# Kernel optimization log

Measured on AMD Instinct MI355X. Metric: run time of the kernel, lower is better.

## Reference

```python
import jax, jax.numpy as jnp
import numpy as np
from jax import lax

T = 256          # sentence length
WD, TD = 300, 100  # word/tag embedding dims
H = WD + TD      # LSTM hidden (=input) size, per module __init__
VOCAB, NTAGS = 50000, 50
MLP_H = 400


def setup_inputs() -> dict:
    key = jax.random.key(0)
    ks = jax.random.split(key, 20)
    s = 0.05  # small init scale for numerical stability
    return {
        "words": jax.random.randint(ks[0], (T,), 0, VOCAB),
        "tags": jax.random.randint(ks[1], (T,), 0, NTAGS),
        "word_emb": jax.random.normal(ks[2], (VOCAB, WD), jnp.float32),
        "tag_emb": jax.random.normal(ks[3], (NTAGS, TD), jnp.float32),
        "Wih0": jax.random.normal(ks[4], (2, 4 * H, H), jnp.float32) * s,
        "Whh0": jax.random.normal(ks[5], (2, 4 * H, H), jnp.float32) * s,
        "bih0": jax.random.normal(ks[6], (2, 4 * H), jnp.float32) * s,
        "bhh0": jax.random.normal(ks[7], (2, 4 * H), jnp.float32) * s,
        "Wih1": jax.random.normal(ks[8], (2, 4 * H, 2 * H), jnp.float32) * s,
        "Whh1": jax.random.normal(ks[9], (2, 4 * H, H), jnp.float32) * s,
        "bih1": jax.random.normal(ks[10], (2, 4 * H), jnp.float32) * s,
        "bhh1": jax.random.normal(ks[11], (2, 4 * H), jnp.float32) * s,
        "W1": jax.random.normal(ks[12], (MLP_H, 4 * H), jnp.float32) * s,
        "b1": jax.random.normal(ks[13], (MLP_H,), jnp.float32) * s,
        "W2": jax.random.normal(ks[14], (1, MLP_H), jnp.float32) * s,
        "b2": jax.random.normal(ks[15], (1,), jnp.float32) * s,
        "h0": jax.random.normal(ks[16], (2, 2, H), jnp.float32),  # [layer, dir, H]
        "c0": jax.random.normal(ks[17], (2, 2, H), jnp.float32),
    }


def _lstm_dir(xs, Wih, Whh, bih, bhh, h0, c0, reverse):
    # xs: [T, D]; torch LSTM gate order i, f, g, o
    def step(carry, xt):
        h, c = carry
        g = xt @ Wih.T + bih + h @ Whh.T + bhh  # [4H]
        i, f, gg, o = jnp.split(g, 4)
        c = jax.nn.sigmoid(f) * c + jax.nn.sigmoid(i) * jnp.tanh(gg)
        h = jax.nn.sigmoid(o) * jnp.tanh(c)
        return (h, c), h
    _, hs = lax.scan(step, (h0, c0), xs, reverse=reverse)
    return hs  # [T, H]


def _forward(words, tags, word_emb, tag_emb, Wih0, Whh0, bih0, bhh0,
             Wih1, Whh1, bih1, bhh1, W1, b1, W2, b2, h0, c0):
    x = jnp.concatenate([word_emb[words], tag_emb[tags]], axis=1)  # [T, H]
    # layer 0, both directions
    hf0 = _lstm_dir(x, Wih0[0], Whh0[0], bih0[0], bhh0[0], h0[0, 0], c0[0, 0], False)
    hb0 = _lstm_dir(x, Wih0[1], Whh0[1], bih0[1], bhh0[1], h0[0, 1], c0[0, 1], True)
    x1 = jnp.concatenate([hf0, hb0], axis=1)  # [T, 2H]
    # layer 1
    hf1 = _lstm_dir(x1, Wih1[0], Whh1[0], bih1[0], bhh1[0], h0[1, 0], c0[1, 0], False)
    hb1 = _lstm_dir(x1, Wih1[1], Whh1[1], bih1[1], bhh1[1], h0[1, 1], c0[1, 1], True)
    hvec = jnp.concatenate([hf1, hb1], axis=1)  # [T, 2H]
    # batched pairwise MLP: score(i,j) = W2 @ tanh(W1 @ [h_i; h_j] + b1) + b2
    # Split W1 so the concat is never materialized over all T^2 pairs.
    W1a, W1b = W1[:, :2 * H], W1[:, 2 * H:]
    pi = hvec @ W1a.T  # [T, MLP_H] contribution of head word i
    pj = hvec @ W1b.T  # [T, MLP_H] contribution of dependent word j
    act = jnp.tanh(pi[:, None, :] + pj[None, :, :] + b1)  # [T, T, MLP_H]
    scores = act @ W2[0] + b2[0]  # [T, T]
    # diagonal stays 0 (permutations exclude i == j; scoreTensor was zeroed)
    return scores * (1.0 - jnp.eye(T, dtype=scores.dtype))


def reference(words, tags, word_emb, tag_emb, Wih0, Whh0, bih0, bhh0,
              Wih1, Whh1, bih1, bhh1, W1, b1, W2, b2, h0, c0):
    return _forward(words, tags, word_emb, tag_emb, Wih0, Whh0, bih0, bhh0,
                    Wih1, Whh1, bih1, bhh1, W1, b1, W2, b2, h0, c0)
```

## Files before the change

kernel.cpp:

```cpp
#include <hip/hip_runtime.h>
#include <hip/hip_bf16.h>

#define T 256
#define H 400
#define G4 1600
#define WD 300
#define TD 100
#define MLP_H 400
#define NBLK_D 25
#define HB 16
#define GR 64
#define WSTR 202
#define NPAIR 200

typedef _Float16 f16;
typedef _Float16 half2t __attribute__((ext_vector_type(2)));
typedef unsigned long long u64;
typedef unsigned int u32;

__device__ __forceinline__ float fexp(float x) {
    return __builtin_amdgcn_exp2f(x * 1.4426950408889634f);
}
__device__ __forceinline__ float sigf(float x) {
    return __builtin_amdgcn_rcpf(1.0f + fexp(-x));
}
__device__ __forceinline__ float tanhf_fast(float x) {
    return 1.0f - 2.0f * __builtin_amdgcn_rcpf(1.0f + fexp(2.0f * x));
}
__device__ __forceinline__ unsigned short f16bits(f16 x) {
    union { f16 h; unsigned short u; } v; v.h = x; return v.u;
}
__device__ __forceinline__ u32 packh2(float a, float b) {
    half2t hv; hv.x = (_Float16)a; hv.y = (_Float16)b;
    return __builtin_bit_cast(u32, hv);
}

#if __has_builtin(__builtin_amdgcn_fdot2)
__device__ __forceinline__ float dot2u(u32 a, u32 b, float c) {
    return __builtin_amdgcn_fdot2(__builtin_bit_cast(half2t, a),
                                  __builtin_bit_cast(half2t, b), c, false);
}
#else
__device__ __forceinline__ float dot2u(u32 a, u32 b, float c) {
    half2t x = __builtin_bit_cast(half2t, a), y = __builtin_bit_cast(half2t, b);
    return fmaf((float)x.y, (float)y.y, fmaf((float)x.x, (float)y.x, c));
}
#endif

__device__ __forceinline__ u64 sysload(const u64* p) {
    return __hip_atomic_load(p, __ATOMIC_RELAXED, __HIP_MEMORY_SCOPE_SYSTEM);
}
__device__ __forceinline__ void sysstore(u64* p, u64 v) {
    __hip_atomic_store(p, v, __ATOMIC_RELAXED, __HIP_MEMORY_SCOPE_SYSTEM);
}

__global__ void gather_k(const int* __restrict__ words, const int* __restrict__ tags,
                         const float* __restrict__ wemb, const float* __restrict__ temb,
                         float* __restrict__ x0) {
    int t = blockIdx.x;
    int w = words[t], g = tags[t];
    for (int c = threadIdx.x; c < H; c += 128) {
        float v = (c < WD) ? wemb[w * WD + c] : temb[g * TD + (c - WD)];
        x0[t * H + c] = v;
    }
}

__global__ __launch_bounds__(256) void gemm_tn(
    const float* __restrict__ X, int ldx,
    const float* __restrict__ Wt, int ldw, int wofs,
    const float* __restrict__ bias1, const float* __restrict__ bias2,
    float* __restrict__ out, int ldo, int Rt, int K) {
    __shared__ float Xs[64][17];
    __shared__ float Ws[64][17];
    const int tid = threadIdx.x;
    const int t0 = blockIdx.x * 64, r0 = blockIdx.y * 64;
    const int lr = tid >> 2, kq = (tid & 3) * 4;
    const int ti = tid >> 4, rj = tid & 15;
    float acc[4][4] = {};
    for (int k0 = 0; k0 < K; k0 += 16) {
        float4 xv = *(const float4*)(X + (size_t)(t0 + lr) * ldx + k0 + kq);
        Xs[lr][kq + 0] = xv.x; Xs[lr][kq + 1] = xv.y;
        Xs[lr][kq + 2] = xv.z; Xs[lr][kq + 3] = xv.w;
        int r = r0 + lr;
        float4 wv = make_float4(0.f, 0.f, 0.f, 0.f);
        if (r < Rt) wv = *(const float4*)(Wt + (size_t)r * ldw + wofs + k0 + kq);
        Ws[lr][kq + 0] = wv.x; Ws[lr][kq + 1] = wv.y;
        Ws[lr][kq + 2] = wv.z; Ws[lr][kq + 3] = wv.w;
        __syncthreads();
#pragma unroll
        for (int k = 0; k < 16; k++) {
            float xr[4], wr[4];
#pragma unroll
            for (int m = 0; m < 4; m++) xr[m] = Xs[ti * 4 + m][k];
#pragma unroll
            for (int n = 0; n < 4; n++) wr[n] = Ws[rj * 4 + n][k];
#pragma unroll
            for (int m = 0; m < 4; m++)
#pragma unroll
                for (int n = 0; n < 4; n++)
                    acc[m][n] = fmaf(xr[m], wr[n], acc[m][n]);
        }
        __syncthreads();
    }
    int rq = r0 + rj * 4;
    if (rq < Rt) {
        float b[4];
#pragma unroll
        for (int n = 0; n < 4; n++) {
            int r = rq + n;
            b[n] = (bias1 ? bias1[r] : 0.f) + (bias2 ? bias2[r] : 0.f);
        }
#pragma unroll
        for (int m = 0; m < 4; m++) {
            int t = t0 + ti * 4 + m;
            float4 o;
            o.x = acc[m][0] + b[0]; o.y = acc[m][1] + b[1];
            o.z = acc[m][2] + b[2]; o.w = acc[m][3] + b[3];
            *(float4*)(out + (size_t)t * ldo + rq) = o;
        }
    }
}

__global__ void lstm_init5(const float* __restrict__ h0, u64* sA, u64* sB) {
    int tid = threadIdx.x;
    const int TOT = 2 * 2 * NPAIR;
    for (int i = tid; i < TOT; i += 256) { sA[i] = 0xFFFFULL; sB[i] = 0xFFFFULL; }
    __syncthreads();
    for (int p = tid; p < 2 * NPAIR; p += 256) {
        int d = p / NPAIR, pr = p - d * NPAIR;
        size_t off = (size_t)(d * 2 + 0) * NPAIR + pr;
        f16 a0 = (f16)h0[d * H + 2 * pr], b0 = (f16)h0[d * H + 2 * pr + 1];
        sA[off] = 0ULL | ((u64)f16bits(a0) << 16) | ((u64)f16bits(b0) << 32);
        f16 a1 = (f16)h0[2 * H + d * H + 2 * pr], b1 = (f16)h0[2 * H + d * H + 2 * pr + 1];
        sB[off] = 0ULL | ((u64)f16bits(a1) << 16) | ((u64)f16bits(b1) << 32);
    }
}

__global__ __launch_bounds__(512, 1) void lstm_layer8(
    const float* __restrict__ G,
    const float* __restrict__ Whh,
    const float* __restrict__ c0l,
    float* __restrict__ xout,
    u64* __restrict__ slots) {
    const int role = blockIdx.x;
    const int dir = role / NBLK_D, blk = role - dir * NBLK_D;
    const int tid = threadIdx.x;
    const float* Wd = Whh + (size_t)dir * G4 * H;
    const float* Gd = G + (size_t)dir * T * G4;
    u64* sd = slots + (size_t)dir * 2 * NPAIR;

    __shared__ u32 wlds[GR * WSTR];
    __shared__ __align__(16) u32 hsh[NPAIR];
    __shared__ float gsum[GR];
    __shared__ float gsh[2][GR];

    for (int idx = tid; idx < GR * 100; idx += 512) {
        int row = idx / 100, c4 = idx - row * 100;
        int g = row >> 4, r = row & 15;
        const float4* src = (const float4*)(Wd + (size_t)(g * H + blk * HB + r) * H);
        float4 f = src[c4];
        *(uint2*)&wlds[row * WSTR + c4 * 2] =
            make_uint2(packh2(f.x, f.y), packh2(f.z, f.w));
    }
    if (tid >= 448) {
        int i = tid - 448, gg = i >> 4, rr = i & 15;
        int tt0 = dir ? (T - 1) : 0;
        gsh[0][i] = Gd[(size_t)tt0 * G4 + gg * H + blk * HB + rr];
    } else if (tid < 8) {
        u64 v = sysload(sd + blk * 8 + tid);
        hsh[blk * 8 + tid] = (u32)(v >> 16);
    }
    float c = (tid < 64) ? c0l[dir * H + blk * HB + (tid & 15)] : 0.f;
    __syncthreads();

#pragma clang loop unroll(disable)
    for (int s = 0; s < T; ++s) {
        if (tid >= 256 && tid < 448) {
            int f = tid - 256;
            int widx = f + (f >= blk * 8 ? 8 : 0);
            u64* src = sd + (size_t)(s & 1) * NPAIR + widx;
            u64 v = sysload(src);
            int spins = 0;
            while ((unsigned)(v & 0xFFFFULL) != (unsigned)s) {
                if (++spins > 16384) {
                    v = __hip_atomic_fetch_add(src, 0ULL, __ATOMIC_RELAXED,
                                               __HIP_MEMORY_SCOPE_AGENT);
                } else {
                    v = sysload(src);
                }
            }
            hsh[widx] = (u32)(v >> 16);
        } else if (tid >= 448) {
            int sn = (s + 1 < T) ? (s + 1) : s;
            int tt = dir ? (T - 1 - sn) : sn;
            int i = tid - 448, gg = i >> 4, rr = i & 15;
            gsh[(s + 1) & 1][i] = Gd[(size_t)tt * G4 + gg * H + blk * HB + rr];
        }
        __syncthreads();

        if (tid < 256) {
            const int row = tid >> 2, sl = tid & 3;
            const u32* wp = &wlds[row * WSTR + sl * 50];
            const u32* hp = &hsh[sl * 50];
            float a0 = 0.f, a1 = 0.f, a2 = 0.f, a3 = 0.f;
#pragma unroll
            for (int i = 0; i < 12; ++i) {
                uint2 wv0 = *(const uint2*)&wp[4 * i];
                uint2 hv0 = *(const uint2*)&hp[4 * i];
                uint2 wv1 = *(const uint2*)&wp[4 * i + 2];
                uint2 hv1 = *(const uint2*)&hp[4 * i + 2];
                a0 = dot2u(wv0.x, hv0.x, a0);
                a1 = dot2u(wv0.y, hv0.y, a1);
                a2 = dot2u(wv1.x, hv1.x, a2);
                a3 = dot2u(wv1.y, hv1.y, a3);
            }
            {
                uint2 wv = *(const uint2*)&wp[48];
                uint2 hv = *(const uint2*)&hp[48];
                a0 = dot2u(wv.x, hv.x, a0);
                a1 = dot2u(wv.y, hv.y, a1);
            }
            float a = (a0 + a1) + (a2 + a3);
            a += __shfl_xor(a, 1);
            a += __shfl_xor(a, 2);
            if (sl == 0) gsum[row] = a;
        }
        __syncthreads();

        if (tid < 64) {
            const int r = tid & 15;
            const float* gc = gsh[s & 1];
            float iv = gsum[r]      + gc[r];
            float fv = gsum[16 + r] + gc[16 + r];
            float gv = gsum[32 + r] + gc[32 + r];
            float ov = gsum[48 + r] + gc[48 + r];
            float cn = sigf(fv) * c + sigf(iv) * tanhf_fast(gv);
            c = cn;
            float hn = sigf(ov) * tanhf_fast(cn);
            u32 hb = (u32)f16bits((f16)hn);
            u32 lo = __shfl(hb, (2 * tid) & 63);
            u32 hi = __shfl(hb, (2 * tid + 1) & 63);
            if (tid < 8) {
                u32 pk = (lo & 0xFFFFu) | (hi << 16);
                hsh[blk * 8 + tid] = pk;
                sysstore(sd + (size_t)((s + 1) & 1) * NPAIR + blk * 8 + tid,
                         (u64)(unsigned)(s + 1) | ((u64)pk << 16));
            }
            const int tt = dir ? (T - 1 - s) : s;
            if (tid < 16)
                xout[(size_t)tt * (2 * H) + dir * H + blk * HB + tid] = hn;
        }
    }
}

__global__ __launch_bounds__(256) void scores_k(
    const float* __restrict__ pi, const float* __restrict__ pj,
    const float* __restrict__ w2, const float* __restrict__ b2p,
    float* __restrict__ out) {
    __shared__ float Ps[16][401];
    __shared__ float Qs[16][401];
    __shared__ float w2s[400];
    const int tid = threadIdx.x;
    const int i0 = blockIdx.y * 16, j0 = blockIdx.x * 16;
    for (int r = 0; r < 16; r++) {
        for (int k = tid; k < MLP_H; k += 256) {
            Ps[r][k] = pi[(size_t)(i0 + r) * MLP_H + k];
            Qs[r][k] = pj[(size_t)(j0 + r) * MLP_H + k];
        }
    }
    for (int k = tid; k < MLP_H; k += 256) w2s[k] = w2[k];
    __syncthreads();
    const int ti = tid >> 4, tj = tid & 15;
    float acc = 0.f;
#pragma unroll 4
    for (int k = 0; k < MLP_H; k++) {
        float x = Ps[ti][k] + Qs[tj][k];
        acc = fmaf(w2s[k], tanhf_fast(x), acc);
    }
    const int i = i0 + ti, j = j0 + tj;
    out[(size_t)i * T + j] = (i == j) ? 0.f : (acc + b2p[0]);
}

extern "C" void kernel_launch(void* const* d_in, const int* in_sizes, int n_in,
                              void* d_out, int out_size, void* d_ws, size_t ws_size,
                              hipStream_t stream) {
    const int*   words = (const int*)d_in[0];
    const int*   tags  = (const int*)d_in[1];
    const float* wemb  = (const float*)d_in[2];
    const float* temb  = (const float*)d_in[3];
    const float* Wih0  = (const float*)d_in[4];
    const float* Whh0  = (const float*)d_in[5];
    const float* bih0  = (const float*)d_in[6];
    const float* bhh0  = (const float*)d_in[7];
    const float* Wih1  = (const float*)d_in[8];
    const float* Whh1  = (const float*)d_in[9];
    const float* bih1  = (const float*)d_in[10];
    const float* bhh1  = (const float*)d_in[11];
    const float* W1    = (const float*)d_in[12];
    const float* b1    = (const float*)d_in[13];
    const float* W2    = (const float*)d_in[14];
    const float* b2    = (const float*)d_in[15];
    const float* h0    = (const float*)d_in[16];
    const float* c0    = (const float*)d_in[17];
    float* out = (float*)d_out;

    float* W = (float*)d_ws;
    float* x0   = W;
    float* x1   = W + 102400;
    float* hvec = W + 307200;
    float* Gb   = W + 512000;
    float* pi   = W + 1331200;
    float* pj   = W + 1433600;
    u64* slotsA = (u64*)W;
    u64* slotsB = (u64*)(W + 2048);

    gather_k<<<T, 128, 0, stream>>>(words, tags, wemb, temb, x0);

    for (int d = 0; d < 2; d++) {
        gemm_tn<<<dim3(4, 25), 256, 0, stream>>>(
            x0, H, Wih0 + (size_t)d * G4 * H, H, 0,
            bih0 + d * G4, bhh0 + d * G4,
            Gb + (size_t)d * T * G4, G4, G4, H);
    }
    lstm_init5<<<1, 256, 0, stream>>>(h0, slotsA, slotsB);
    lstm_layer8<<<2 * NBLK_D, 512, 0, stream>>>(Gb, Whh0, c0, x1, slotsA);

    for (int d = 0; d < 2; d++) {
        gemm_tn<<<dim3(4, 25), 256, 0, stream>>>(
            x1, 2 * H, Wih1 + (size_t)d * G4 * (2 * H), 2 * H, 0,
            bih1 + d * G4, bhh1 + d * G4,
            Gb + (size_t)d * T * G4, G4, G4, 2 * H);
    }
    lstm_layer8<<<2 * NBLK_D, 512, 0, stream>>>(Gb, Whh1, c0 + 2 * H, hvec, slotsB);

    gemm_tn<<<dim3(4, 7), 256, 0, stream>>>(
        hvec, 2 * H, W1, G4, 0, b1, nullptr, pi, MLP_H, MLP_H, 2 * H);
    gemm_tn<<<dim3(4, 7), 256, 0, stream>>>(
        hvec, 2 * H, W1, G4, 2 * H, nullptr, nullptr, pj, MLP_H, MLP_H, 2 * H);

    scores_k<<<dim3(16, 16), 256, 0, stream>>>(pi, pj, W2, b2, out);
}
```

Baseline: 1.436 ms.

## Interleave forward and backward LSTM directions in one block to hide sync latency

Each of 25 blocks now holds Whh slices for both directions and alternates forward and backward half-steps inside one loop. While one direction computes, the spin-wait for the other direction's hidden state from peer blocks runs, so cross-block exchange latency overlaps with compute. This halves the block count and doubles LDS weight storage per block. It also serializes the two directions' compute within a block and adds barriers per step.

```diff
diff --git a/kernel.cpp b/kernel.cpp
--- a/kernel.cpp
+++ b/kernel.cpp
@@ -7,7 +7,7 @@
 #define WD 300
 #define TD 100
 #define MLP_H 400
-#define NBLK_D 25
+#define NBLK 25
 #define HB 16
 #define GR 64
 #define WSTR 202
@@ -136,119 +136,146 @@
     }
 }
 
-__global__ __launch_bounds__(512, 1) void lstm_layer8(
+__global__ __launch_bounds__(512, 1) void lstm_layer_dual(
     const float* __restrict__ G,
     const float* __restrict__ Whh,
     const float* __restrict__ c0l,
     float* __restrict__ xout,
     u64* __restrict__ slots) {
-    const int role = blockIdx.x;
-    const int dir = role / NBLK_D, blk = role - dir * NBLK_D;
+    const int blk = blockIdx.x;
     const int tid = threadIdx.x;
-    const float* Wd = Whh + (size_t)dir * G4 * H;
-    const float* Gd = G + (size_t)dir * T * G4;
-    u64* sd = slots + (size_t)dir * 2 * NPAIR;
-
-    __shared__ u32 wlds[GR * WSTR];
-    __shared__ __align__(16) u32 hsh[NPAIR];
+    u64* sdF = slots;
+    u64* sdB = slots + 2 * NPAIR;
+
+    __shared__ u32 wlds[2][GR * WSTR];
+    __shared__ __align__(16) u32 hshF[NPAIR];
+    __shared__ __align__(16) u32 hshB[NPAIR];
     __shared__ float gsum[GR];
-    __shared__ float gsh[2][GR];
-
-    for (int idx = tid; idx < GR * 100; idx += 512) {
-        int row = idx / 100, c4 = idx - row * 100;
+    __shared__ float gshF[2][GR];
+    __shared__ float gshB[2][GR];
+
+    for (int idx = tid; idx < 2 * GR * 100; idx += 512) {
+        int d = idx / (GR * 100), rem = idx - d * (GR * 100);
+        int row = rem / 100, c4 = rem - row * 100;
         int g = row >> 4, r = row & 15;
-        const float4* src = (const float4*)(Wd + (size_t)(g * H + blk * HB + r) * H);
+        const float4* src = (const float4*)(
+            Whh + (size_t)d * G4 * H + (size_t)(g * H + blk * HB + r) * H);
         float4 f = src[c4];
-        *(uint2*)&wlds[row * WSTR + c4 * 2] =
+        *(uint2*)&wlds[d][row * WSTR + c4 * 2] =
             make_uint2(packh2(f.x, f.y), packh2(f.z, f.w));
     }
     if (tid >= 448) {
         int i = tid - 448, gg = i >> 4, rr = i & 15;
-        int tt0 = dir ? (T - 1) : 0;
-        gsh[0][i] = Gd[(size_t)tt0 * G4 + gg * H + blk * HB + rr];
+        gshF[0][i] = G[(size_t)0 * G4 + gg * H + blk * HB + rr];
+        gshB[0][i] = G[((size_t)T + (T - 1)) * G4 + gg * H + blk * HB + rr];
     } else if (tid < 8) {
-        u64 v = sysload(sd + blk * 8 + tid);
-        hsh[blk * 8 + tid] = (u32)(v >> 16);
-    }
-    float c = (tid < 64) ? c0l[dir * H + blk * HB + (tid & 15)] : 0.f;
+        u64 v = sysload(sdF + blk * 8 + tid);
+        hshF[blk * 8 + tid] = (u32)(v >> 16);
+    } else if (tid < 16) {
+        u64 v = sysload(sdB + blk * 8 + (tid - 8));
+        hshB[blk * 8 + (tid - 8)] = (u32)(v >> 16);
+    } else if (tid >= 256 && tid < 448) {
+        int f = tid - 256;
+        int widx = f + (f >= blk * 8 ? 8 : 0);
+        u64* src = sdF + widx;
+        u64 v = sysload(src);
+        int spins = 0;
+        while ((unsigned)(v & 0xFFFFULL) != 0u) {
+            if (++spins > 16384) {
+                v = __hip_atomic_fetch_add(src, 0ULL, __ATOMIC_RELAXED,
+                                           __HIP_MEMORY_SCOPE_AGENT);
+            } else {
+                v = sysload(src);
+            }
+        }
+        hshF[widx] = (u32)(v >> 16);
+    }
+    float cf = (tid < 64) ? c0l[blk * HB + (tid & 15)] : 0.f;
+    float cb = (tid < 64) ? c0l[H + blk * HB + (tid & 15)] : 0.f;
     __syncthreads();
 
 #pragma clang loop unroll(disable)
     for (int s = 0; s < T; ++s) {
-        if (tid >= 256 && tid < 448) {
-            int f = tid - 256;
-            int widx = f + (f >= blk * 8 ? 8 : 0);
-            u64* src = sd + (size_t)(s & 1) * NPAIR + widx;
-            u64 v = sysload(src);
-            int spins = 0;
-            while ((unsigned)(v & 0xFFFFULL) != (unsigned)s) {
-                if (++spins > 16384) {
-                    v = __hip_atomic_fetch_add(src, 0ULL, __ATOMIC_RELAXED,
-                                               __HIP_MEMORY_SCOPE_AGENT);
-                } else {
-                    v = sysload(src);
+#pragma clang loop unroll(disable)
+        for (int d = 0; d < 2; ++d) {
+            if (tid >= 256 && tid < 448) {
+                int f = tid - 256;
+                int widx = f + (f >= blk * 8 ? 8 : 0);
+                int tg = (d == 0) ? s : (s + 1);
+                if (tg < T) {
+                    u64* src = (d == 0 ? sdB : sdF) + (size_t)(tg & 1) * NPAIR + widx;
+                    u64 v = sysload(src);
+                    int spins = 0;
+                    while ((unsigned)(v & 0xFFFFULL) != (unsigned)tg) {
+                        if (++spins > 16384) {
+                            v = __hip_atomic_fetch_add(src, 0ULL, __ATOMIC_RELAXED,
+                                                       __HIP_MEMORY_SCOPE_AGENT);
+                        } else {
+                            v = sysload(src);
+                        }
+                    }
+                    (d == 0 ? hshB : hshF)[widx] = (u32)(v >> 16);
                 }
+            } else if (tid >= 448) {
+                int sn = (s + 1 < T) ? (s + 1) : s;
+                int tt = d ? (T - 1 - sn) : sn;
+                int i = tid - 448, gg = i >> 4, rr = i & 15;
+                (d ? gshB : gshF)[(s + 1) & 1][i] =
+                    G[((size_t)d * T + tt) * G4 + gg * H + blk * HB + rr];
+            } else {
+                const int row = tid >> 2, sl = tid & 3;
+                const u32* wp = &wlds[d][row * WSTR + sl * 50];
+                const u32* hp = &(d ? hshB : hshF)[sl * 50];
+                float a0 = 0.f, a1 = 0.f, a2 = 0.f, a3 = 0.f;
+#pragma unroll
+                for (int i = 0; i < 12; ++i) {
+                    uint2 wv0 = *(const uint2*)&wp[4 * i];
+                    uint2 hv0 = *(const uint2*)&hp[4 * i];
+                    uint2 wv1 = *(const uint2*)&wp[4 * i + 2];
+                    uint2 hv1 = *(const uint2*)&hp[4 * i + 2];
+                    a0 = dot2u(wv0.x, hv0.x, a0);
+                    a1 = dot2u(wv0.y, hv0.y, a1);
+                    a2 = dot2u(wv1.x, hv1.x, a2);
+                    a3 = dot2u(wv1.y, hv1.y, a3);
+                }
+                {
+                    uint2 wv = *(const uint2*)&wp[48];
+                    uint2 hv = *(const uint2*)&hp[48];
+                    a0 = dot2u(wv.x, hv.x, a0);
+                    a1 = dot2u(wv.y, hv.y, a1);
+                }
+                float a = (a0 + a1) + (a2 + a3);
+                a += __shfl_xor(a, 1);
+                a += __shfl_xor(a, 2);
+                if (sl == 0) gsum[row] = a;
             }
-            hsh[widx] = (u32)(v >> 16);
-        } else if (tid >= 448) {
-            int sn = (s + 1 < T) ? (s + 1) : s;
-            int tt = dir ? (T - 1 - sn) : sn;
-            int i = tid - 448, gg = i >> 4, rr = i & 15;
-            gsh[(s + 1) & 1][i] = Gd[(size_t)tt * G4 + gg * H + blk * HB + rr];
-        }
-        __syncthreads();
-
-        if (tid < 256) {
-            const int row = tid >> 2, sl = tid & 3;
-            const u32* wp = &wlds[row * WSTR + sl * 50];
-            const u32* hp = &hsh[sl * 50];
-            float a0 = 0.f, a1 = 0.f, a2 = 0.f, a3 = 0.f;
-#pragma unroll
-            for (int i = 0; i < 12; ++i) {
-                uint2 wv0 = *(const uint2*)&wp[4 * i];
-                uint2 hv0 = *(const uint2*)&hp[4 * i];
-                uint2 wv1 = *(const uint2*)&wp[4 * i + 2];
-                uint2 hv1 = *(const uint2*)&hp[4 * i + 2];
-                a0 = dot2u(wv0.x, hv0.x, a0);
-                a1 = dot2u(wv0.y, hv0.y, a1);
-                a2 = dot2u(wv1.x, hv1.x, a2);
-                a3 = dot2u(wv1.y, hv1.y, a3);
+            __syncthreads();
+
+            if (tid < 64) {
+                const int r = tid & 15;
+                const float* gc = (d ? gshB : gshF)[s & 1];
+                float iv = gsum[r]      + gc[r];
+                float fv = gsum[16 + r] + gc[16 + r];
+                float gv = gsum[32 + r] + gc[32 + r];
+                float ov = gsum[48 + r] + gc[48 + r];
+                float c = d ? cb : cf;
+                float cn = sigf(fv) * c + sigf(iv) * tanhf_fast(gv);
+                if (d) cb = cn; else cf = cn;
+                float hn = sigf(ov) * tanhf_fast(cn);
+                u32 hb = (u32)f16bits((f16)hn);
+                u32 lo = __shfl(hb, (2 * tid) & 63);
+                u32 hi = __shfl(hb, (2 * tid + 1) & 63);
+                if (tid < 8) {
+                    u32 pk = (lo & 0xFFFFu) | (hi << 16);
+                    (d ? hshB : hshF)[blk * 8 + tid] = pk;
+                    sysstore((d ? sdB : sdF) + (size_t)((s + 1) & 1) * NPAIR + blk * 8 + tid,
+                             (u64)(unsigned)(s + 1) | ((u64)pk << 16));
+                }
+                const int tt = d ? (T - 1 - s) : s;
+                if (tid < 16)
+                    xout[(size_t)tt * (2 * H) + d * H + blk * HB + tid] = hn;
             }
-            {
-                uint2 wv = *(const uint2*)&wp[48];
-                uint2 hv = *(const uint2*)&hp[48];
-                a0 = dot2u(wv.x, hv.x, a0);
-                a1 = dot2u(wv.y, hv.y, a1);
-            }
-            float a = (a0 + a1) + (a2 + a3);
-            a += __shfl_xor(a, 1);
-            a += __shfl_xor(a, 2);
-            if (sl == 0) gsum[row] = a;
-        }
-        __syncthreads();
-
-        if (tid < 64) {
-            const int r = tid & 15;
-            const float* gc = gsh[s & 1];
-            float iv = gsum[r]      + gc[r];
-            float fv = gsum[16 + r] + gc[16 + r];
-            float gv = gsum[32 + r] + gc[32 + r];
-            float ov = gsum[48 + r] + gc[48 + r];
-            float cn = sigf(fv) * c + sigf(iv) * tanhf_fast(gv);
-            c = cn;
-            float hn = sigf(ov) * tanhf_fast(cn);
-            u32 hb = (u32)f16bits((f16)hn);
-            u32 lo = __shfl(hb, (2 * tid) & 63);
-            u32 hi = __shfl(hb, (2 * tid + 1) & 63);
-            if (tid < 8) {
-                u32 pk = (lo & 0xFFFFu) | (hi << 16);
-                hsh[blk * 8 + tid] = pk;
-                sysstore(sd + (size_t)((s + 1) & 1) * NPAIR + blk * 8 + tid,
-                         (u64)(unsigned)(s + 1) | ((u64)pk << 16));
-            }
-            const int tt = dir ? (T - 1 - s) : s;
-            if (tid < 16)
-                xout[(size_t)tt * (2 * H) + dir * H + blk * HB + tid] = hn;
+            __syncthreads();
         }
     }
 }
@@ -323,7 +350,7 @@
             Gb + (size_t)d * T * G4, G4, G4, H);
     }
     lstm_init5<<<1, 256, 0, stream>>>(h0, slotsA, slotsB);
-    lstm_layer8<<<2 * NBLK_D, 512, 0, stream>>>(Gb, Whh0, c0, x1, slotsA);
+    lstm_layer_dual<<<NBLK, 512, 0, stream>>>(Gb, Whh0, c0, x1, slotsA);
 
     for (int d = 0; d < 2; d++) {
         gemm_tn<<<dim3(4, 25), 256, 0, stream>>>(
@@ -331,7 +358,7 @@
             bih1 + d * G4, bhh1 + d * G4,
             Gb + (size_t)d * T * G4, G4, G4, 2 * H);
     }
-    lstm_layer8<<<2 * NBLK_D, 512, 0, stream>>>(Gb, Whh1, c0 + 2 * H, hvec, slotsB);
+    lstm_layer_dual<<<NBLK, 512, 0, stream>>>(Gb, Whh1, c0 + 2 * H, hvec, slotsB);
 
     gemm_tn<<<dim3(4, 7), 256, 0, stream>>>(
         hvec, 2 * H, W1, G4, 0, b1, nullptr, pi, MLP_H, MLP_H, 2 * H);
```

After: 1.536 ms. 1.07x slower.
